# Kernel optimization log

Measured on AMD Instinct MI355X. Metric: run time of the kernel, lower is better.

Reference implementation:

```python
import jax, jax.numpy as jnp
import numpy as np
from jax import lax


def setup_inputs() -> dict:
    key = jax.random.key(0)
    k1, k2, k3 = jax.random.split(key, 3)
    B, C, H, W = 16, 64, 128, 128
    Hc = 64
    x = jax.random.normal(k1, (B, C, H, W), dtype=jnp.float32)
    # Conv2d(in=C, out=4*Hc, kernel=(3,1)) weight [O, I, kH, kW] and bias
    fan_in = C * 3 * 1
    bound = 1.0 / np.sqrt(fan_in)
    conv_w = jax.random.uniform(k2, (4 * Hc, C, 3, 1), dtype=jnp.float32, minval=-bound, maxval=bound)
    conv_b = jax.random.uniform(k3, (4 * Hc,), dtype=jnp.float32, minval=-bound, maxval=bound)
    return {"x": x, "conv_w": conv_w, "conv_b": conv_b}


def reference(x, conv_w, conv_b):
    # Gates depend only on x, so run the causal (3,1) conv once over the full image.
    # Top-pad height by 2 (matches F.pad(col, (0,0,2,0)) per column in the original).
    gates = lax.conv_general_dilated(
        x, conv_w,
        window_strides=(1, 1),
        padding=[(2, 0), (0, 0)],
        dimension_numbers=("NCHW", "OIHW", "NCHW"),
    ) + conv_b[None, :, None, None]            # [B, 4*Hc, H, W]

    i, f, o, g = jnp.split(gates, 4, axis=1)   # each [B, Hc, H, W]
    i = jax.nn.sigmoid(i)
    f = jax.nn.sigmoid(f)
    o = jax.nn.sigmoid(o)
    g = jnp.tanh(g)

    # Scan the LSTM cell recurrence over the width dimension.
    # Move W to the leading axis: [W, B, Hc, H]
    seq = tuple(jnp.moveaxis(t, 3, 0) for t in (i, f, o, g))
    Hc = i.shape[1]
    c0 = jnp.zeros((x.shape[0], Hc, x.shape[2]), dtype=x.dtype)

    def step(c, ifog):
        i_t, f_t, o_t, g_t = ifog
        c = f_t * c + i_t * g_t
        h = o_t * jnp.tanh(c)
        return c, h

    _, hs = lax.scan(step, c0, seq)            # hs: [W, B, Hc, H]
    return jnp.moveaxis(hs, 0, 3)              # [B, Hc, H, W]
```

## Files before the change

kernel.cpp:

```cpp
#include <hip/hip_runtime.h>


#define NB   16
#define NC   64
#define NH   128
#define NW   128
#define NHC  64
#define NK   192
#define NPLN (NB * NH * NW * NHC)

typedef _Float16 half4 __attribute__((ext_vector_type(4)));
typedef _Float16 half8 __attribute__((ext_vector_type(8)));
typedef float    f32x4 __attribute__((ext_vector_type(4)));

__device__ __forceinline__ float frcp(float x)  { return __builtin_amdgcn_rcpf(x); }
__device__ __forceinline__ float fsig(float x)  { return frcp(1.f + __expf(-x)); }
__device__ __forceinline__ float ftanh(float x) { return 1.f - 2.f * frcp(__expf(2.f * x) + 1.f); }

#define NIP 3088

__global__ __launch_bounds__(256, 2) void gates_k(
    const float* __restrict__ x,
    const float* __restrict__ wgt,
    const float* __restrict__ bias,
    _Float16* __restrict__ fpl,
    _Float16* __restrict__ ppl,
    _Float16* __restrict__ opl)
{
    __shared__ _Float16 xsf[8 * NIP];

    const int tid  = threadIdx.x;
    const int cg   = tid >> 6;
    const int lane = tid & 63;
    const int l15  = lane & 15;
    const int l4   = lane >> 4;

    int bid = blockIdx.x;
    bid = (bid & 7) * (NB * NH / 8) + (bid >> 3);
    const int b = bid >> 7;
    const int h = bid & (NH - 1);

    const float* xb = x + (size_t)b * NC * NH * NW;

    half8 afrag[4][6];
    #pragma unroll
    for (int g = 0; g < 4; ++g) {
        const float* wo = wgt + (size_t)(g * 64 + cg * 16 + l15) * NK;
        #pragma unroll
        for (int kt = 0; kt < 6; ++kt) {
            const float4 v0 = *(const float4*)(wo + kt * 32 + l4 * 8);
            const float4 v1 = *(const float4*)(wo + kt * 32 + l4 * 8 + 4);
            half8 a;
            a[0] = (_Float16)v0.x; a[1] = (_Float16)v0.y;
            a[2] = (_Float16)v0.z; a[3] = (_Float16)v0.w;
            a[4] = (_Float16)v1.x; a[5] = (_Float16)v1.y;
            a[6] = (_Float16)v1.z; a[7] = (_Float16)v1.w;
            afrag[g][kt] = a;
        }
    }
    float bfr[4][4];
    #pragma unroll
    for (int g = 0; g < 4; ++g)
        #pragma unroll
        for (int j = 0; j < 4; ++j)
            bfr[g][j] = bias[g * 64 + cg * 16 + l4 * 4 + j];

    for (int t = tid; t < 1536; t += 256) {
        const int kq  = t >> 5;
        const int wq  = t & 31;
        const int k0  = kq * 4;
        const int w0g = wq * 4;
        float4 v[4];
        #pragma unroll
        for (int dk = 0; dk < 4; ++dk) {
            const int k  = k0 + dk;
            const int c  = k / 3;
            const int kh = k - 3 * c;
            const int r  = h - 2 + kh;
            v[dk] = (r >= 0) ? *(const float4*)(xb + ((size_t)c * NH + r) * NW + w0g)
                             : make_float4(0.f, 0.f, 0.f, 0.f);
        }
        const int kt = k0 >> 5;
        const int j0 = k0 & 7;
        #pragma unroll
        for (int dw = 0; dw < 4; ++dw) {
            const int w  = w0g + dw;
            const int ni = w >> 4;
            const int L  = ((k0 & 31) >> 3) * 16 + (w & 15);
            half4 hv;
            hv[0] = (_Float16)(&v[0].x)[dw];
            hv[1] = (_Float16)(&v[1].x)[dw];
            hv[2] = (_Float16)(&v[2].x)[dw];
            hv[3] = (_Float16)(&v[3].x)[dw];
            *(half4*)&xsf[ni * NIP + kt * 512 + L * 8 + j0] = hv;
        }
    }
    __syncthreads();

    #pragma unroll
    for (int pr = 0; pr < 4; ++pr) {
        f32x4 acc[4][2];
        #pragma unroll
        for (int g = 0; g < 4; ++g) {
            acc[g][0] = (f32x4){0.f, 0.f, 0.f, 0.f};
            acc[g][1] = (f32x4){0.f, 0.f, 0.f, 0.f};
        }
        #pragma unroll
        for (int kt = 0; kt < 6; ++kt) {
            const half8 b0 = *(const half8*)&xsf[(pr * 2 + 0) * NIP + kt * 512 + lane * 8];
            const half8 b1 = *(const half8*)&xsf[(pr * 2 + 1) * NIP + kt * 512 + lane * 8];
            #pragma unroll
            for (int g = 0; g < 4; ++g) {
                acc[g][0] = __builtin_amdgcn_mfma_f32_16x16x32_f16(afrag[g][kt], b0, acc[g][0], 0, 0, 0);
                acc[g][1] = __builtin_amdgcn_mfma_f32_16x16x32_f16(afrag[g][kt], b1, acc[g][1], 0, 0, 0);
            }
        }
        #pragma unroll
        for (int q = 0; q < 2; ++q) {
            const int w   = (pr * 2 + q) * 16 + l15;
            const int hc0 = cg * 16 + l4 * 4;
            half4 f4, p4, o4;
            #pragma unroll
            for (int j = 0; j < 4; ++j) {
                const float iv = fsig (acc[0][q][j] + bfr[0][j]);
                const float fv = fsig (acc[1][q][j] + bfr[1][j]);
                const float ov = fsig (acc[2][q][j] + bfr[2][j]);
                const float gv = ftanh(acc[3][q][j] + bfr[3][j]);
                f4[j] = (_Float16)fv;
                p4[j] = (_Float16)(iv * gv);
                o4[j] = (_Float16)ov;
            }
            const size_t sb = (((size_t)(b * NH + h) * NW) + w) * NHC + hc0;
            *(half4*)(fpl + sb) = f4;
            *(half4*)(ppl + sb) = p4;
            *(half4*)(opl + sb) = o4;
        }
    }
}

__global__ __launch_bounds__(256) void scan_k(
    const _Float16* __restrict__ fpl,
    const _Float16* __restrict__ ppl,
    const _Float16* __restrict__ opl,
    float* __restrict__ out)
{
    __shared__ float hbuf[4][NHC][33];

    const int tid  = threadIdx.x;
    const int wv   = tid >> 6;
    const int lane = tid & 63;
    const int row  = blockIdx.x * 4 + wv;
    const int b    = row >> 7;
    const int h    = row & (NH - 1);

    const size_t gbase = ((size_t)(b * NH + h) * NW) * NHC + lane;
    float c = 0.f;

    for (int ck = 0; ck < 4; ++ck) {
        const size_t p0 = gbase + (size_t)ck * 32 * NHC;
        #pragma unroll
        for (int s = 0; s < 32; ++s) {
            const size_t ix = p0 + (size_t)s * NHC;
            const float f = (float)fpl[ix];
            const float p = (float)ppl[ix];
            const float o = (float)opl[ix];
            c = fmaf(f, c, p);
            hbuf[wv][lane][s] = o * ftanh(c);
        }
        const int wl = lane & 31;
        const int hq = lane >> 5;
        #pragma unroll
        for (int it = 0; it < 32; ++it) {
            const int hc = it * 2 + hq;
            out[(((size_t)b * NHC + hc) * NH + h) * NW + ck * 32 + wl] = hbuf[wv][hc][wl];
        }
    }
}

#define WC 32
#define GP (WC + 2)
#define NQ (48 * WC)
__device__ __forceinline__ void stage_chunk_fb(const float* __restrict__ xb, int h, int w0,
                                               _Float16 (*xsf)[6][64][8], int qstart, int qstep) {
    for (int q = qstart; q < NQ; q += qstep) {
        const int k4 = q >> 5; const int w = q & 31;
        const int ni = w >> 4; const int kt = k4 >> 3;
        const int L = ((k4 >> 1) & 3) * 16 + (w & 15);
        const int j0 = (k4 & 1) * 4;
        half4 hv;
        #pragma unroll
        for (int e = 0; e < 4; ++e) {
            const int k = k4 * 4 + e; const int c = k / 3;
            const int kh = k - 3 * c; const int r = h - 2 + kh;
            float v = 0.f;
            if (r >= 0) v = xb[((size_t)c * NH + r) * NW + w0 + w];
            hv[e] = (_Float16)v;
        }
        *(half4*)&xsf[ni][kt][L][j0] = hv;
    }
}
__global__ __launch_bounds__(256, 2) void rowlstm_fb(
    const float* __restrict__ x, const float* __restrict__ wgt,
    const float* __restrict__ bias, float* __restrict__ out)
{
    __shared__ _Float16 xsf[2][6][64][8];
    __shared__ float fbuf[NHC][GP]; __shared__ float pbuf[NHC][GP]; __shared__ float obuf[NHC][GP];
    const int tid = threadIdx.x; const int cg = tid >> 6;
    const int lane = tid & 63; const int l15 = lane & 15; const int l4 = lane >> 4;
    int bid = blockIdx.x; bid = (bid & 7) * (NB * NH / 8) + (bid >> 3);
    const int b = bid >> 7; const int h = bid & (NH - 1);
    const float* xb = x + (size_t)b * NC * NH * NW;
    half8 afrag[4][6];
    #pragma unroll
    for (int g = 0; g < 4; ++g) {
        const float* wo = wgt + (size_t)(g * 64 + cg * 16 + l15) * NK;
        #pragma unroll
        for (int kt = 0; kt < 6; ++kt) {
            const float4 v0 = *(const float4*)(wo + kt * 32 + l4 * 8);
            const float4 v1 = *(const float4*)(wo + kt * 32 + l4 * 8 + 4);
            half8 a;
            a[0]=(_Float16)v0.x;a[1]=(_Float16)v0.y;a[2]=(_Float16)v0.z;a[3]=(_Float16)v0.w;
            a[4]=(_Float16)v1.x;a[5]=(_Float16)v1.y;a[6]=(_Float16)v1.z;a[7]=(_Float16)v1.w;
            afrag[g][kt] = a;
        }
    }
    float bfr[4][4];
    #pragma unroll
    for (int g = 0; g < 4; ++g)
        #pragma unroll
        for (int j = 0; j < 4; ++j) bfr[g][j] = bias[g * 64 + cg * 16 + l4 * 4 + j];
    float cstate = 0.f;
    float* outrow = out + (((size_t)b * NHC + tid) * NH + h) * NW;
    stage_chunk_fb(xb, h, 0, xsf, tid, 256);
    __syncthreads();
    for (int ck = 0; ck < 4; ++ck) {
        const int w0 = ck * WC;
        f32x4 acc[4][2];
        #pragma unroll
        for (int g = 0; g < 4; ++g) { acc[g][0]=(f32x4){0,0,0,0}; acc[g][1]=(f32x4){0,0,0,0}; }
        #pragma unroll
        for (int kt = 0; kt < 6; ++kt) {
            const half8 b0 = *(const half8*)&xsf[0][kt][lane][0];
            const half8 b1 = *(const half8*)&xsf[1][kt][lane][0];
            #pragma unroll
            for (int g = 0; g < 4; ++g) {
                acc[g][0] = __builtin_amdgcn_mfma_f32_16x16x32_f16(afrag[g][kt], b0, acc[g][0], 0, 0, 0);
                acc[g][1] = __builtin_amdgcn_mfma_f32_16x16x32_f16(afrag[g][kt], b1, acc[g][1], 0, 0, 0);
            }
        }
        #pragma unroll
        for (int ni = 0; ni < 2; ++ni)
            #pragma unroll
            for (int j = 0; j < 4; ++j) {
                const float iv = fsig (acc[0][ni][j] + bfr[0][j]);
                const float fv = fsig (acc[1][ni][j] + bfr[1][j]);
                const float ov = fsig (acc[2][ni][j] + bfr[2][j]);
                const float gv = ftanh(acc[3][ni][j] + bfr[3][j]);
                const int hcr = cg * 16 + l4 * 4 + j; const int wcl = ni * 16 + l15;
                fbuf[hcr][wcl] = fv; pbuf[hcr][wcl] = iv * gv; obuf[hcr][wcl] = ov;
            }
        __syncthreads();
        if (tid < 64) {
            float c = cstate;
            #pragma unroll
            for (int w = 0; w < WC; w += 4) {
                float4 hv;
                #pragma unroll
                for (int e = 0; e < 4; ++e) {
                    c = fmaf(fbuf[tid][w + e], c, pbuf[tid][w + e]);
                    (&hv.x)[e] = obuf[tid][w + e] * ftanh(c);
                }
                *(float4*)(outrow + w0 + w) = hv;
            }
            cstate = c;
        } else if (ck < 3) stage_chunk_fb(xb, h, w0 + WC, xsf, tid - 64, 192);
        __syncthreads();
    }
}

extern "C" void kernel_launch(void* const* d_in, const int* in_sizes, int n_in,
                              void* d_out, int out_size, void* d_ws, size_t ws_size,
                              hipStream_t stream) {
    const float* x    = (const float*)d_in[0];
    const float* wgt  = (const float*)d_in[1];
    const float* bias = (const float*)d_in[2];
    float* out = (float*)d_out;

    if (ws_size >= (size_t)3 * NPLN * sizeof(_Float16)) {
        _Float16* fpl = (_Float16*)d_ws;
        _Float16* ppl = fpl + NPLN;
        _Float16* opl = ppl + NPLN;
        gates_k<<<NB * NH, 256, 0, stream>>>(x, wgt, bias, fpl, ppl, opl);
        scan_k<<<NB * NH / 4, 256, 0, stream>>>(fpl, ppl, opl, out);
    } else {
        rowlstm_fb<<<NB * NH, 256, 0, stream>>>(x, wgt, bias, out);
    }
}
```

Baseline: 262.3 us.

## Parallelize LSTM width scan across waves and process two rows per gates block

```diff
diff --git a/kernel.cpp b/kernel.cpp
--- a/kernel.cpp
+++ b/kernel.cpp
@@ -36,9 +36,9 @@
     const int l4   = lane >> 4;
 
     int bid = blockIdx.x;
-    bid = (bid & 7) * (NB * NH / 8) + (bid >> 3);
-    const int b = bid >> 7;
-    const int h = bid & (NH - 1);
+    bid = (bid & 7) * (1024 / 8) + (bid >> 3);
+    const int b  = bid >> 6;
+    const int h0 = (bid & 63) * 2;
 
     const float* xb = x + (size_t)b * NC * NH * NW;
 
@@ -65,115 +65,141 @@
         for (int j = 0; j < 4; ++j)
             bfr[g][j] = bias[g * 64 + cg * 16 + l4 * 4 + j];
 
-    for (int t = tid; t < 1536; t += 256) {
-        const int kq  = t >> 5;
-        const int wq  = t & 31;
-        const int k0  = kq * 4;
-        const int w0g = wq * 4;
-        float4 v[4];
-        #pragma unroll
-        for (int dk = 0; dk < 4; ++dk) {
-            const int k  = k0 + dk;
-            const int c  = k / 3;
-            const int kh = k - 3 * c;
-            const int r  = h - 2 + kh;
-            v[dk] = (r >= 0) ? *(const float4*)(xb + ((size_t)c * NH + r) * NW + w0g)
-                             : make_float4(0.f, 0.f, 0.f, 0.f);
-        }
-        const int kt = k0 >> 5;
-        const int j0 = k0 & 7;
-        #pragma unroll
-        for (int dw = 0; dw < 4; ++dw) {
-            const int w  = w0g + dw;
-            const int ni = w >> 4;
-            const int L  = ((k0 & 31) >> 3) * 16 + (w & 15);
-            half4 hv;
-            hv[0] = (_Float16)(&v[0].x)[dw];
-            hv[1] = (_Float16)(&v[1].x)[dw];
-            hv[2] = (_Float16)(&v[2].x)[dw];
-            hv[3] = (_Float16)(&v[3].x)[dw];
-            *(half4*)&xsf[ni * NIP + kt * 512 + L * 8 + j0] = hv;
-        }
-    }
-    __syncthreads();
-
-    #pragma unroll
-    for (int pr = 0; pr < 4; ++pr) {
-        f32x4 acc[4][2];
-        #pragma unroll
-        for (int g = 0; g < 4; ++g) {
-            acc[g][0] = (f32x4){0.f, 0.f, 0.f, 0.f};
-            acc[g][1] = (f32x4){0.f, 0.f, 0.f, 0.f};
-        }
-        #pragma unroll
-        for (int kt = 0; kt < 6; ++kt) {
-            const half8 b0 = *(const half8*)&xsf[(pr * 2 + 0) * NIP + kt * 512 + lane * 8];
-            const half8 b1 = *(const half8*)&xsf[(pr * 2 + 1) * NIP + kt * 512 + lane * 8];
+    for (int hh = 0; hh < 2; ++hh) {
+        const int h = h0 + hh;
+
+        for (int t = tid; t < 1536; t += 256) {
+            const int kq  = t >> 5;
+            const int wq  = t & 31;
+            const int k0  = kq * 4;
+            const int w0g = wq * 4;
+            float4 v[4];
+            #pragma unroll
+            for (int dk = 0; dk < 4; ++dk) {
+                const int k  = k0 + dk;
+                const int c  = k / 3;
+                const int kh = k - 3 * c;
+                const int r  = h - 2 + kh;
+                v[dk] = (r >= 0) ? *(const float4*)(xb + ((size_t)c * NH + r) * NW + w0g)
+                                 : make_float4(0.f, 0.f, 0.f, 0.f);
+            }
+            const int kt = k0 >> 5;
+            const int j0 = k0 & 7;
+            #pragma unroll
+            for (int dw = 0; dw < 4; ++dw) {
+                const int w  = w0g + dw;
+                const int ni = w >> 4;
+                const int L  = ((k0 & 31) >> 3) * 16 + (w & 15);
+                half4 hv;
+                hv[0] = (_Float16)(&v[0].x)[dw];
+                hv[1] = (_Float16)(&v[1].x)[dw];
+                hv[2] = (_Float16)(&v[2].x)[dw];
+                hv[3] = (_Float16)(&v[3].x)[dw];
+                *(half4*)&xsf[ni * NIP + kt * 512 + L * 8 + j0] = hv;
+            }
+        }
+        __syncthreads();
+
+        #pragma unroll
+        for (int pr = 0; pr < 4; ++pr) {
+            f32x4 acc[4][2];
             #pragma unroll
             for (int g = 0; g < 4; ++g) {
-                acc[g][0] = __builtin_amdgcn_mfma_f32_16x16x32_f16(afrag[g][kt], b0, acc[g][0], 0, 0, 0);
-                acc[g][1] = __builtin_amdgcn_mfma_f32_16x16x32_f16(afrag[g][kt], b1, acc[g][1], 0, 0, 0);
-            }
-        }
-        #pragma unroll
-        for (int q = 0; q < 2; ++q) {
-            const int w   = (pr * 2 + q) * 16 + l15;
-            const int hc0 = cg * 16 + l4 * 4;
-            half4 f4, p4, o4;
-            #pragma unroll
-            for (int j = 0; j < 4; ++j) {
-                const float iv = fsig (acc[0][q][j] + bfr[0][j]);
-                const float fv = fsig (acc[1][q][j] + bfr[1][j]);
-                const float ov = fsig (acc[2][q][j] + bfr[2][j]);
-                const float gv = ftanh(acc[3][q][j] + bfr[3][j]);
-                f4[j] = (_Float16)fv;
-                p4[j] = (_Float16)(iv * gv);
-                o4[j] = (_Float16)ov;
-            }
-            const size_t sb = (((size_t)(b * NH + h) * NW) + w) * NHC + hc0;
-            *(half4*)(fpl + sb) = f4;
-            *(half4*)(ppl + sb) = p4;
-            *(half4*)(opl + sb) = o4;
-        }
-    }
-}
-
-__global__ __launch_bounds__(256) void scan_k(
+                acc[g][0] = (f32x4){0.f, 0.f, 0.f, 0.f};
+                acc[g][1] = (f32x4){0.f, 0.f, 0.f, 0.f};
+            }
+            #pragma unroll
+            for (int kt = 0; kt < 6; ++kt) {
+                const half8 b0 = *(const half8*)&xsf[(pr * 2 + 0) * NIP + kt * 512 + lane * 8];
+                const half8 b1 = *(const half8*)&xsf[(pr * 2 + 1) * NIP + kt * 512 + lane * 8];
+                #pragma unroll
+                for (int g = 0; g < 4; ++g) {
+                    acc[g][0] = __builtin_amdgcn_mfma_f32_16x16x32_f16(afrag[g][kt], b0, acc[g][0], 0, 0, 0);
+                    acc[g][1] = __builtin_amdgcn_mfma_f32_16x16x32_f16(afrag[g][kt], b1, acc[g][1], 0, 0, 0);
+                }
+            }
+            #pragma unroll
+            for (int q = 0; q < 2; ++q) {
+                const int w   = (pr * 2 + q) * 16 + l15;
+                const int hc0 = cg * 16 + l4 * 4;
+                half4 f4, p4, o4;
+                #pragma unroll
+                for (int j = 0; j < 4; ++j) {
+                    const float iv = fsig (acc[0][q][j] + bfr[0][j]);
+                    const float fv = fsig (acc[1][q][j] + bfr[1][j]);
+                    const float ov = fsig (acc[2][q][j] + bfr[2][j]);
+                    const float gv = ftanh(acc[3][q][j] + bfr[3][j]);
+                    f4[j] = (_Float16)fv;
+                    p4[j] = (_Float16)(iv * gv);
+                    o4[j] = (_Float16)ov;
+                }
+                const size_t sb = (((size_t)(b * NH + h) * NW) + w) * NHC + hc0;
+                *(half4*)(fpl + sb) = f4;
+                *(half4*)(ppl + sb) = p4;
+                *(half4*)(opl + sb) = o4;
+            }
+        }
+        __syncthreads();
+    }
+}
+
+__global__ __launch_bounds__(256, 4) void scan_k(
     const _Float16* __restrict__ fpl,
     const _Float16* __restrict__ ppl,
     const _Float16* __restrict__ opl,
     float* __restrict__ out)
 {
+    __shared__ float AB[4][NHC][2];
     __shared__ float hbuf[4][NHC][33];
 
     const int tid  = threadIdx.x;
     const int wv   = tid >> 6;
     const int lane = tid & 63;
-    const int row  = blockIdx.x * 4 + wv;
+    const int row  = blockIdx.x;
     const int b    = row >> 7;
     const int h    = row & (NH - 1);
-
-    const size_t gbase = ((size_t)(b * NH + h) * NW) * NHC + lane;
+    const int w0   = wv * 32;
+
+    const size_t gbase = (((size_t)(b * NH + h) * NW) + w0) * NHC + lane;
+
+    _Float16 fu[32], pu[32];
+    #pragma unroll
+    for (int s = 0; s < 32; ++s) {
+        fu[s] = fpl[gbase + (size_t)s * NHC];
+        pu[s] = ppl[gbase + (size_t)s * NHC];
+    }
+    float A = 1.f, Bv = 0.f;
+    #pragma unroll
+    for (int s = 0; s < 32; ++s) {
+        const float f = (float)fu[s];
+        A  = A * f;
+        Bv = fmaf(f, Bv, (float)pu[s]);
+    }
+    AB[wv][lane][0] = A;
+    AB[wv][lane][1] = Bv;
+    __syncthreads();
+
     float c = 0.f;
-
-    for (int ck = 0; ck < 4; ++ck) {
-        const size_t p0 = gbase + (size_t)ck * 32 * NHC;
-        #pragma unroll
-        for (int s = 0; s < 32; ++s) {
-            const size_t ix = p0 + (size_t)s * NHC;
-            const float f = (float)fpl[ix];
-            const float p = (float)ppl[ix];
-            const float o = (float)opl[ix];
-            c = fmaf(f, c, p);
-            hbuf[wv][lane][s] = o * ftanh(c);
-        }
-        const int wl = lane & 31;
-        const int hq = lane >> 5;
-        #pragma unroll
-        for (int it = 0; it < 32; ++it) {
-            const int hc = it * 2 + hq;
-            out[(((size_t)b * NHC + hc) * NH + h) * NW + ck * 32 + wl] = hbuf[wv][hc][wl];
-        }
+    for (int s = 0; s < wv; ++s)
+        c = fmaf(AB[s][lane][0], c, AB[s][lane][1]);
+
+    _Float16 ou[32];
+    #pragma unroll
+    for (int s = 0; s < 32; ++s)
+        ou[s] = opl[gbase + (size_t)s * NHC];
+
+    #pragma unroll
+    for (int s = 0; s < 32; ++s) {
+        c = fmaf((float)fu[s], c, (float)pu[s]);
+        hbuf[wv][lane][s] = (float)ou[s] * ftanh(c);
+    }
+
+    const int wl = lane & 31;
+    const int hq = lane >> 5;
+    #pragma unroll
+    for (int it = 0; it < 32; ++it) {
+        const int hc = it * 2 + hq;
+        out[(((size_t)b * NHC + hc) * NH + h) * NW + w0 + wl] = hbuf[wv][hc][wl];
     }
 }
 
@@ -290,8 +316,8 @@
         _Float16* fpl = (_Float16*)d_ws;
         _Float16* ppl = fpl + NPLN;
         _Float16* opl = ppl + NPLN;
-        gates_k<<<NB * NH, 256, 0, stream>>>(x, wgt, bias, fpl, ppl, opl);
-        scan_k<<<NB * NH / 4, 256, 0, stream>>>(fpl, ppl, opl, out);
+        gates_k<<<1024, 256, 0, stream>>>(x, wgt, bias, fpl, ppl, opl);
+        scan_k<<<NB * NH, 256, 0, stream>>>(fpl, ppl, opl, out);
     } else {
         rowlstm_fb<<<NB * NH, 256, 0, stream>>>(x, wgt, bias, out);
     }
```

Result: faster. 224.3 us (-14.5%).
